# Optimization experiments

Hardware: AMD Instinct MI355X
Metric: run time of the kernel (lower is better)

Reference implementation:

```python
import jax, jax.numpy as jnp
import numpy as np

# irreps_in = irreps_out = 256x0e + 128x1o + 64x2e
MULS = [256, 128, 64]      # multiplicities per irrep
IRDIMS = [1, 3, 5]          # 2l+1 for l=0,1,2
N = 200000                  # number of atoms / nodes
DIM = sum(m * d for m, d in zip(MULS, IRDIMS))          # 960
WNUM = sum(m * m for m in MULS)                          # 86016
BNUM = MULS[0]                                           # bias only on scalar (0e) outputs


def setup_inputs() -> dict:
    key = jax.random.key(0)
    k1, k2, k3 = jax.random.split(key, 3)
    x = jax.random.normal(k1, (N, DIM), dtype=jnp.float32)
    w = jax.random.normal(k2, (WNUM,), dtype=jnp.float32)
    b = jax.random.normal(k3, (BNUM,), dtype=jnp.float32) * 0.1
    return {"x": x, "w": w, "b": b}


def reference(x, w, b):
    # Faithful to _codegen_linear with f_in=f_out=None, shared_weights=True:
    # per-irrep block einsum 'uw,zui->zwi' scaled by 1/sqrt(mul_in), plus bias on 0e block.
    n = x.shape[0]
    outs = []
    xoff = 0
    woff = 0
    for mul, d in zip(MULS, IRDIMS):
        blk = x[:, xoff:xoff + mul * d].reshape(n, mul, d)          # (N, u, i)
        W = w[woff:woff + mul * mul].reshape(mul, mul)              # (u, w)
        pw = mul ** -0.5                                            # path_weight (element norm)
        o = pw * jnp.einsum('uw,nui->nwi', W, blk)                  # (N, w, i)
        o = o.reshape(n, mul * d)
        if d == 1:  # scalar irrep: bias path, path_weight = 1
            o = o + b.reshape(1, mul)
        outs.append(o)
        xoff += mul * d
        woff += mul * mul
    return jnp.concatenate(outs, axis=-1)  # (N, 960)
```

## Files before the change

kernel.cpp:

```cpp
#include <hip/hip_runtime.h>


typedef short frag8 __attribute__((ext_vector_type(8)));
typedef float f32x4 __attribute__((ext_vector_type(4)));
typedef unsigned int u32;
typedef u32 u32x4 __attribute__((ext_vector_type(4)));

static __device__ __forceinline__ short f2bf(float f) {
    union { float f; unsigned u; } v; v.f = f;
    unsigned r = (v.u + 0x7FFFu + ((v.u >> 16) & 1u)) >> 16;
    return (short)r;
}

static __device__ __forceinline__ u32 cvtpk(float lo, float hi) {
    u32 r;
    asm("v_cvt_pk_bf16_f32 %0, %1, %2" : "=v"(r) : "v"(lo), "v"(hi));
    return r;
}

static __device__ __forceinline__ frag8 asfrag(u32x4 u) {
    union { u32x4 u; frag8 f; } t; t.u = u; return t.f;
}

#define MFMA(a, b, c) __builtin_amdgcn_mfma_f32_16x16x32_bf16((a), (b), (c), 0, 0, 0)

__global__ __launch_bounds__(256) void prep_kernel(const float* __restrict__ w,
                                                   short* __restrict__ wf) {
    int e = blockIdx.x * 256 + threadIdx.x;
    int f = e >> 9;
    int r = e & 511;
    int l = r >> 3, j = r & 7;
    int l15 = l & 15, lg = l >> 4;
    int kk = 4 * lg + (j & 3) + 16 * (j >> 2);
    int u, wc, woff, mul; float scale;
    if (f < 128) {
        int nt = f >> 3, s = f & 7;
        u = 32 * s + kk; wc = nt * 16 + l15; woff = 0;     mul = 256; scale = 0.0625f;
    } else if (f < 160) {
        int g = f - 128, nt = g >> 2, s = g & 3;
        u = 32 * s + kk; wc = nt * 16 + l15; woff = 65536; mul = 128; scale = 0.088388347648318447f;
    } else {
        int g = f - 160, nt = g >> 1, s = g & 1;
        u = 32 * s + kk; wc = nt * 16 + l15; woff = 81920; mul = 64;  scale = 0.125f;
    }
    wf[e] = f2bf(scale * w[woff + u * mul + wc]);
}

static __device__ __forceinline__ void gload_lds16(const void* g, void* l) {
    __builtin_amdgcn_global_load_lds(
        (const __attribute__((address_space(1))) unsigned int*)g,
        (__attribute__((address_space(3))) unsigned int*)l, 16, 0, 0);
}

__global__ __launch_bounds__(256) void lin_tile(const float* __restrict__ x,
                                                const short* __restrict__ wf,
                                                const float* __restrict__ bias,
                                                float* __restrict__ out) {
    __shared__ __align__(16) char smem[24576];
    const int tid  = threadIdx.x;
    const int lane = tid & 63;
    const int wv   = tid >> 6;
    const int l15  = lane & 15;
    const int lg   = lane >> 4;
    const int fam  = blockIdx.y;
    const long rowbase = (long)blockIdx.x * 16;
    const char* __restrict__ xb = (const char*)x + rowbase * 3840;
    char* __restrict__ ob = (char*)out + rowbase * 3840;
    const frag8* __restrict__ wfr = (const frag8*)wf;
    const int sw4 = (l15 & 7) << 4;

    if (fam == 0) {
        #pragma unroll
        for (int j = 0; j < 4; ++j) {
            int c  = j * 256 + tid;
            int r  = c >> 6;
            int cc = c & 63;
            int g  = cc ^ (r & 7);
            gload_lds16(xb + r * 3840 + (g << 4),
                        smem + (j * 256 + wv * 64) * 16);
        }
    } else if (fam == 1) {
        #pragma unroll
        for (int j = 0; j < 6; ++j) {
            int c  = j * 256 + tid;
            int r  = c / 96;
            int cc = c - r * 96;
            int g  = cc ^ (r & 7);
            gload_lds16(xb + r * 3840 + 1024 + (g << 4),
                        smem + (j * 256 + wv * 64) * 16);
        }
    } else {
        #pragma unroll
        for (int j = 0; j < 5; ++j) {
            int c  = j * 256 + tid;
            int r  = c / 80;
            int cc = c - r * 80;
            int g  = cc ^ (r & 7);
            gload_lds16(xb + r * 3840 + 2560 + (g << 4),
                        smem + (j * 256 + wv * 64) * 16);
        }
    }
    __syncthreads();

    if (fam == 0) {
        const char* sb = smem + l15 * 1024;
        #define LDC0(cc) (*(const f32x4*)(sb + (((cc) << 4) ^ sw4)))
        frag8 a0[8];
        #pragma unroll
        for (int s = 0; s < 8; ++s) {
            const f32x4 v0 = LDC0(8 * s + lg);
            const f32x4 v1 = LDC0(8 * s + 4 + lg);
            u32x4 t = { cvtpk(v0[0], v0[1]), cvtpk(v0[2], v0[3]),
                        cvtpk(v1[0], v1[1]), cvtpk(v1[2], v1[3]) };
            a0[s] = asfrag(t);
        }
        #undef LDC0
        f32x4 st[4];
        #pragma unroll
        for (int q = 0; q < 4; ++q) {
            const int nt = 4 * wv + q;
            f32x4 acc = {0.f, 0.f, 0.f, 0.f};
            #pragma unroll
            for (int s = 0; s < 8; ++s) {
                frag8 bw = wfr[(nt * 8 + s) * 64 + lane];
                acc = MFMA(bw, a0[s], acc);
            }
            const f32x4 bv = *(const f32x4*)(bias + nt * 16 + 4 * lg);
            st[q][0] = acc[0] + bv[0]; st[q][1] = acc[1] + bv[1];
            st[q][2] = acc[2] + bv[2]; st[q][3] = acc[3] + bv[3];
        }
        __syncthreads();
        #pragma unroll
        for (int q = 0; q < 4; ++q) {
            const int g0 = (4 * wv + q) * 4 + lg;
            *(f32x4*)(smem + l15 * 1024 + (((g0 ^ (l15 & 7))) << 4)) = st[q];
        }
        __syncthreads();
        #pragma unroll
        for (int j = 0; j < 4; ++j) {
            int c = j * 256 + tid;
            int r = c >> 6;
            int g = c & 63;
            f32x4 v = *(const f32x4*)(smem + r * 1024 + ((g ^ (r & 7)) << 4));
            *(f32x4*)(ob + (long)r * 3840 + (g << 4)) = v;
        }
    } else if (fam == 1) {
        const char* sb = smem + l15 * 1536;
        #define LDC1(cc) (*(const f32x4*)(sb + (((cc) << 4) ^ sw4)))
        u32x4 a1u[12];
        #pragma unroll
        for (int s = 0; s < 4; ++s) {
            #pragma unroll
            for (int h = 0; h < 2; ++h) {
                const int cb = 24 * s + 12 * h + 3 * lg;
                const f32x4 q0 = LDC1(cb);
                const f32x4 q1 = LDC1(cb + 1);
                const f32x4 q2 = LDC1(cb + 2);
                a1u[0 + s][2 * h]     = cvtpk(q0[0], q0[3]);
                a1u[0 + s][2 * h + 1] = cvtpk(q1[2], q2[1]);
                a1u[4 + s][2 * h]     = cvtpk(q0[1], q1[0]);
                a1u[4 + s][2 * h + 1] = cvtpk(q1[3], q2[2]);
                a1u[8 + s][2 * h]     = cvtpk(q0[2], q1[1]);
                a1u[8 + s][2 * h + 1] = cvtpk(q2[0], q2[3]);
            }
        }
        #undef LDC1
        f32x4 sv[2][3];
        #pragma unroll
        for (int q = 0; q < 2; ++q) {
            const int nt = 2 * wv + q;
            f32x4 c0 = {0.f,0.f,0.f,0.f}, c1 = {0.f,0.f,0.f,0.f}, c2 = {0.f,0.f,0.f,0.f};
            #pragma unroll
            for (int s = 0; s < 4; ++s) {
                frag8 bw = wfr[(128 + nt * 4 + s) * 64 + lane];
                c0 = MFMA(bw, asfrag(a1u[0 + s]), c0);
                c1 = MFMA(bw, asfrag(a1u[4 + s]), c1);
                c2 = MFMA(bw, asfrag(a1u[8 + s]), c2);
            }
            sv[q][0] = (f32x4){c0[0], c1[0], c2[0], c0[1]};
            sv[q][1] = (f32x4){c1[1], c2[1], c0[2], c1[2]};
            sv[q][2] = (f32x4){c2[2], c0[3], c1[3], c2[3]};
        }
        __syncthreads();
        #pragma unroll
        for (int q = 0; q < 2; ++q) {
            const int g0 = 3 * ((2 * wv + q) * 4 + lg);
            char* wb = smem + l15 * 1536;
            #pragma unroll
            for (int i = 0; i < 3; ++i)
                *(f32x4*)(wb + (((g0 + i) ^ (l15 & 7)) << 4)) = sv[q][i];
        }
        __syncthreads();
        #pragma unroll
        for (int j = 0; j < 6; ++j) {
            int c = j * 256 + tid;
            int r = c / 96;
            int g = c - r * 96;
            f32x4 v = *(const f32x4*)(smem + r * 1536 + ((g ^ (r & 7)) << 4));
            *(f32x4*)(ob + (long)r * 3840 + 1024 + (g << 4)) = v;
        }
    } else {
        const char* sb = smem + l15 * 1280;
        #define LDC2(cc) (*(const f32x4*)(sb + (((cc) << 4) ^ sw4)))
        u32x4 a2u[10];
        #pragma unroll
        for (int s = 0; s < 2; ++s) {
            #pragma unroll
            for (int h = 0; h < 2; ++h) {
                const int cb = 40 * s + 20 * h + 5 * lg;
                const f32x4 q0 = LDC2(cb);
                const f32x4 q1 = LDC2(cb + 1);
                const f32x4 q2 = LDC2(cb + 2);
                const f32x4 q3 = LDC2(cb + 3);
                const f32x4 q4 = LDC2(cb + 4);
                a2u[0 + s][2 * h]     = cvtpk(q0[0], q1[1]);
                a2u[0 + s][2 * h + 1] = cvtpk(q2[2], q3[3]);
                a2u[2 + s][2 * h]     = cvtpk(q0[1], q1[2]);
                a2u[2 + s][2 * h + 1] = cvtpk(q2[3], q4[0]);
                a2u[4 + s][2 * h]     = cvtpk(q0[2], q1[3]);
                a2u[4 + s][2 * h + 1] = cvtpk(q3[0], q4[1]);
                a2u[6 + s][2 * h]     = cvtpk(q0[3], q2[0]);
                a2u[6 + s][2 * h + 1] = cvtpk(q3[1], q4[2]);
                a2u[8 + s][2 * h]     = cvtpk(q1[0], q2[1]);
                a2u[8 + s][2 * h + 1] = cvtpk(q3[2], q4[3]);
            }
        }
        #undef LDC2
        f32x4 sv[5];
        {
            const int nt = wv;
            f32x4 c0 = {0.f,0.f,0.f,0.f}, c1 = {0.f,0.f,0.f,0.f}, c2 = {0.f,0.f,0.f,0.f},
                  c3 = {0.f,0.f,0.f,0.f}, c4 = {0.f,0.f,0.f,0.f};
            #pragma unroll
            for (int s = 0; s < 2; ++s) {
                frag8 bw = wfr[(160 + nt * 2 + s) * 64 + lane];
                c0 = MFMA(bw, asfrag(a2u[0 + s]), c0);
                c1 = MFMA(bw, asfrag(a2u[2 + s]), c1);
                c2 = MFMA(bw, asfrag(a2u[4 + s]), c2);
                c3 = MFMA(bw, asfrag(a2u[6 + s]), c3);
                c4 = MFMA(bw, asfrag(a2u[8 + s]), c4);
            }
            sv[0] = (f32x4){c0[0], c1[0], c2[0], c3[0]};
            sv[1] = (f32x4){c4[0], c0[1], c1[1], c2[1]};
            sv[2] = (f32x4){c3[1], c4[1], c0[2], c1[2]};
            sv[3] = (f32x4){c2[2], c3[2], c4[2], c0[3]};
            sv[4] = (f32x4){c1[3], c2[3], c3[3], c4[3]};
        }
        __syncthreads();
        {
            const int g0 = 5 * (wv * 4 + lg);
            char* wb = smem + l15 * 1280;
            #pragma unroll
            for (int i = 0; i < 5; ++i)
                *(f32x4*)(wb + (((g0 + i) ^ (l15 & 7)) << 4)) = sv[i];
        }
        __syncthreads();
        #pragma unroll
        for (int j = 0; j < 5; ++j) {
            int c = j * 256 + tid;
            int r = c / 80;
            int g = c - r * 80;
            f32x4 v = *(const f32x4*)(smem + r * 1280 + ((g ^ (r & 7)) << 4));
            *(f32x4*)(ob + (long)r * 3840 + 2560 + (g << 4)) = v;
        }
    }
}

extern "C" void kernel_launch(void* const* d_in, const int* in_sizes, int n_in,
                              void* d_out, int out_size, void* d_ws, size_t ws_size,
                              hipStream_t stream) {
    const float* x = (const float*)d_in[0];
    const float* w = (const float*)d_in[1];
    const float* b = (const float*)d_in[2];
    float* out = (float*)d_out;
    short* wf  = (short*)d_ws;

    hipLaunchKernelGGL(prep_kernel, dim3(336), dim3(256), 0, stream, w, wf);
    hipLaunchKernelGGL(lin_tile, dim3(12500, 3), dim3(256), 0, stream,
                       x, wf, b, out);
}
```

Measured before the change: 353.7 us.

## Make blocks persistent over five row tiles with double-buffered async LDS prefetch

Each block now handles five consecutive 16-row tiles instead of one, and prefetches the next tile into a second LDS buffer with global_load_lds while computing the current one. Output staging moves to a separate LDS region. Bias and weight fragments are hoisted into registers once per block. The aim is to overlap global loads with MFMA work and to amortise block launch and weight loads, at the cost of 72KB of dynamic LDS per block, which sharply lowers resident blocks per CU.

```diff
diff --git a/kernel.cpp b/kernel.cpp
--- a/kernel.cpp
+++ b/kernel.cpp
@@ -5,6 +5,8 @@
 typedef float f32x4 __attribute__((ext_vector_type(4)));
 typedef unsigned int u32;
 typedef u32 u32x4 __attribute__((ext_vector_type(4)));
+
+#define TILE_B 61440L
 
 static __device__ __forceinline__ short f2bf(float f) {
     union { float f; unsigned u; } v; v.f = f;
@@ -52,216 +54,251 @@
         (__attribute__((address_space(3))) unsigned int*)l, 16, 0, 0);
 }
 
-__global__ __launch_bounds__(256) void lin_tile(const float* __restrict__ x,
+__global__ __launch_bounds__(256) void lin_pipe(const float* __restrict__ x,
                                                 const short* __restrict__ wf,
                                                 const float* __restrict__ bias,
                                                 float* __restrict__ out) {
-    __shared__ __align__(16) char smem[24576];
+    extern __shared__ __align__(16) char smem[];
     const int tid  = threadIdx.x;
     const int lane = tid & 63;
     const int wv   = tid >> 6;
     const int l15  = lane & 15;
     const int lg   = lane >> 4;
+    const int sw4  = (l15 & 7) << 4;
     const int fam  = blockIdx.y;
-    const long rowbase = (long)blockIdx.x * 16;
-    const char* __restrict__ xb = (const char*)x + rowbase * 3840;
-    char* __restrict__ ob = (char*)out + rowbase * 3840;
+    const long tile0 = (long)blockIdx.x * 5;
+    const char* __restrict__ xbase = (const char*)x;
+    char* __restrict__ obase = (char*)out;
     const frag8* __restrict__ wfr = (const frag8*)wf;
-    const int sw4 = (l15 & 7) << 4;
 
     if (fam == 0) {
-        #pragma unroll
-        for (int j = 0; j < 4; ++j) {
-            int c  = j * 256 + tid;
-            int r  = c >> 6;
-            int cc = c & 63;
-            int g  = cc ^ (r & 7);
-            gload_lds16(xb + r * 3840 + (g << 4),
-                        smem + (j * 256 + wv * 64) * 16);
+        f32x4 bv[4];
+        #pragma unroll
+        for (int q = 0; q < 4; ++q)
+            bv[q] = *(const f32x4*)(bias + (4 * wv + q) * 16 + 4 * lg);
+        {
+            const char* xb = xbase + tile0 * TILE_B;
+            #pragma unroll
+            for (int j = 0; j < 4; ++j) {
+                int c = j * 256 + tid, r = c >> 6, g = (c & 63) ^ (r & 7);
+                gload_lds16(xb + r * 3840 + (g << 4), smem + (j * 256 + wv * 64) * 16);
+            }
+        }
+        __syncthreads();
+        #pragma unroll
+        for (int it = 0; it < 5; ++it) {
+            const long tile = tile0 + it;
+            const int cur = it & 1;
+            if (it < 4) {
+                const char* xb = xbase + (tile + 1) * TILE_B;
+                char* db = smem + (cur ^ 1) * 16384;
+                #pragma unroll
+                for (int j = 0; j < 4; ++j) {
+                    int c = j * 256 + tid, r = c >> 6, g = (c & 63) ^ (r & 7);
+                    gload_lds16(xb + r * 3840 + (g << 4), db + (j * 256 + wv * 64) * 16);
+                }
+            }
+            const char* sb = smem + cur * 16384 + l15 * 1024;
+            frag8 a0[8];
+            #pragma unroll
+            for (int s = 0; s < 8; ++s) {
+                const f32x4 v0 = *(const f32x4*)(sb + (((8 * s + lg) << 4) ^ sw4));
+                const f32x4 v1 = *(const f32x4*)(sb + (((8 * s + 4 + lg) << 4) ^ sw4));
+                u32x4 t = { cvtpk(v0[0], v0[1]), cvtpk(v0[2], v0[3]),
+                            cvtpk(v1[0], v1[1]), cvtpk(v1[2], v1[3]) };
+                a0[s] = asfrag(t);
+            }
+            f32x4 st[4];
+            #pragma unroll
+            for (int q = 0; q < 4; ++q) {
+                const int nt = 4 * wv + q;
+                f32x4 acc = {0.f, 0.f, 0.f, 0.f};
+                #pragma unroll
+                for (int s = 0; s < 8; ++s)
+                    acc = MFMA(wfr[(nt * 8 + s) * 64 + lane], a0[s], acc);
+                st[q] = acc + bv[q];
+            }
+            #pragma unroll
+            for (int q = 0; q < 4; ++q) {
+                const int g0 = (4 * wv + q) * 4 + lg;
+                *(f32x4*)(smem + 32768 + l15 * 1024 + ((g0 ^ (l15 & 7)) << 4)) = st[q];
+            }
+            __syncthreads();
+            char* ob = obase + tile * TILE_B;
+            #pragma unroll
+            for (int j = 0; j < 4; ++j) {
+                int c = j * 256 + tid, r = c >> 6, g = c & 63;
+                f32x4 v = *(const f32x4*)(smem + 32768 + r * 1024 + ((g ^ (r & 7)) << 4));
+                *(f32x4*)(ob + (long)r * 3840 + (g << 4)) = v;
+            }
+            __syncthreads();
         }
     } else if (fam == 1) {
-        #pragma unroll
-        for (int j = 0; j < 6; ++j) {
-            int c  = j * 256 + tid;
-            int r  = c / 96;
-            int cc = c - r * 96;
-            int g  = cc ^ (r & 7);
-            gload_lds16(xb + r * 3840 + 1024 + (g << 4),
-                        smem + (j * 256 + wv * 64) * 16);
+        frag8 w1[8];
+        #pragma unroll
+        for (int q = 0; q < 2; ++q)
+            #pragma unroll
+            for (int s = 0; s < 4; ++s)
+                w1[q * 4 + s] = wfr[(128 + (2 * wv + q) * 4 + s) * 64 + lane];
+        {
+            const char* xb = xbase + tile0 * TILE_B;
+            #pragma unroll
+            for (int j = 0; j < 6; ++j) {
+                int c = j * 256 + tid, r = c / 96, cc = c - r * 96, g = cc ^ (r & 7);
+                gload_lds16(xb + r * 3840 + 1024 + (g << 4), smem + (j * 256 + wv * 64) * 16);
+            }
+        }
+        __syncthreads();
+        #pragma unroll
+        for (int it = 0; it < 5; ++it) {
+            const long tile = tile0 + it;
+            const int cur = it & 1;
+            if (it < 4) {
+                const char* xb = xbase + (tile + 1) * TILE_B;
+                char* db = smem + (cur ^ 1) * 24576;
+                #pragma unroll
+                for (int j = 0; j < 6; ++j) {
+                    int c = j * 256 + tid, r = c / 96, cc = c - r * 96, g = cc ^ (r & 7);
+                    gload_lds16(xb + r * 3840 + 1024 + (g << 4), db + (j * 256 + wv * 64) * 16);
+                }
+            }
+            const char* sb = smem + cur * 24576 + l15 * 1536;
+            u32x4 a1u[12];
+            #pragma unroll
+            for (int s = 0; s < 4; ++s) {
+                #pragma unroll
+                for (int h = 0; h < 2; ++h) {
+                    const int cb = 24 * s + 12 * h + 3 * lg;
+                    const f32x4 q0 = *(const f32x4*)(sb + ((cb << 4) ^ sw4));
+                    const f32x4 q1 = *(const f32x4*)(sb + (((cb + 1) << 4) ^ sw4));
+                    const f32x4 q2 = *(const f32x4*)(sb + (((cb + 2) << 4) ^ sw4));
+                    a1u[0 + s][2 * h]     = cvtpk(q0[0], q0[3]);
+                    a1u[0 + s][2 * h + 1] = cvtpk(q1[2], q2[1]);
+                    a1u[4 + s][2 * h]     = cvtpk(q0[1], q1[0]);
+                    a1u[4 + s][2 * h + 1] = cvtpk(q1[3], q2[2]);
+                    a1u[8 + s][2 * h]     = cvtpk(q0[2], q1[1]);
+                    a1u[8 + s][2 * h + 1] = cvtpk(q2[0], q2[3]);
+                }
+            }
+            f32x4 sv[2][3];
+            #pragma unroll
+            for (int q = 0; q < 2; ++q) {
+                f32x4 c0 = {0.f,0.f,0.f,0.f}, c1 = {0.f,0.f,0.f,0.f}, c2 = {0.f,0.f,0.f,0.f};
+                #pragma unroll
+                for (int s = 0; s < 4; ++s) {
+                    frag8 bw = w1[q * 4 + s];
+                    c0 = MFMA(bw, asfrag(a1u[0 + s]), c0);
+                    c1 = MFMA(bw, asfrag(a1u[4 + s]), c1);
+                    c2 = MFMA(bw, asfrag(a1u[8 + s]), c2);
+                }
+                sv[q][0] = (f32x4){c0[0], c1[0], c2[0], c0[1]};
+                sv[q][1] = (f32x4){c1[1], c2[1], c0[2], c1[2]};
+                sv[q][2] = (f32x4){c2[2], c0[3], c1[3], c2[3]};
+            }
+            #pragma unroll
+            for (int q = 0; q < 2; ++q) {
+                const int g0 = 3 * ((2 * wv + q) * 4 + lg);
+                char* wb = smem + 49152 + l15 * 1536;
+                #pragma unroll
+                for (int i = 0; i < 3; ++i)
+                    *(f32x4*)(wb + (((g0 + i) ^ (l15 & 7)) << 4)) = sv[q][i];
+            }
+            __syncthreads();
+            char* ob = obase + tile * TILE_B;
+            #pragma unroll
+            for (int j = 0; j < 6; ++j) {
+                int c = j * 256 + tid, r = c / 96, g = c - r * 96;
+                f32x4 v = *(const f32x4*)(smem + 49152 + r * 1536 + ((g ^ (r & 7)) << 4));
+                *(f32x4*)(ob + (long)r * 3840 + 1024 + (g << 4)) = v;
+            }
+            __syncthreads();
         }
     } else {
-        #pragma unroll
-        for (int j = 0; j < 5; ++j) {
-            int c  = j * 256 + tid;
-            int r  = c / 80;
-            int cc = c - r * 80;
-            int g  = cc ^ (r & 7);
-            gload_lds16(xb + r * 3840 + 2560 + (g << 4),
-                        smem + (j * 256 + wv * 64) * 16);
-        }
-    }
-    __syncthreads();
-
-    if (fam == 0) {
-        const char* sb = smem + l15 * 1024;
-        #define LDC0(cc) (*(const f32x4*)(sb + (((cc) << 4) ^ sw4)))
-        frag8 a0[8];
-        #pragma unroll
-        for (int s = 0; s < 8; ++s) {
-            const f32x4 v0 = LDC0(8 * s + lg);
-            const f32x4 v1 = LDC0(8 * s + 4 + lg);
-            u32x4 t = { cvtpk(v0[0], v0[1]), cvtpk(v0[2], v0[3]),
-                        cvtpk(v1[0], v1[1]), cvtpk(v1[2], v1[3]) };
-            a0[s] = asfrag(t);
-        }
-        #undef LDC0
-        f32x4 st[4];
-        #pragma unroll
-        for (int q = 0; q < 4; ++q) {
-            const int nt = 4 * wv + q;
-            f32x4 acc = {0.f, 0.f, 0.f, 0.f};
-            #pragma unroll
-            for (int s = 0; s < 8; ++s) {
-                frag8 bw = wfr[(nt * 8 + s) * 64 + lane];
-                acc = MFMA(bw, a0[s], acc);
-            }
-            const f32x4 bv = *(const f32x4*)(bias + nt * 16 + 4 * lg);
-            st[q][0] = acc[0] + bv[0]; st[q][1] = acc[1] + bv[1];
-            st[q][2] = acc[2] + bv[2]; st[q][3] = acc[3] + bv[3];
+        frag8 w2[2];
+        #pragma unroll
+        for (int s = 0; s < 2; ++s)
+            w2[s] = wfr[(160 + wv * 2 + s) * 64 + lane];
+        {
+            const char* xb = xbase + tile0 * TILE_B;
+            #pragma unroll
+            for (int j = 0; j < 5; ++j) {
+                int c = j * 256 + tid, r = c / 80, cc = c - r * 80, g = cc ^ (r & 7);
+                gload_lds16(xb + r * 3840 + 2560 + (g << 4), smem + (j * 256 + wv * 64) * 16);
+            }
         }
         __syncthreads();
         #pragma unroll
-        for (int q = 0; q < 4; ++q) {
-            const int g0 = (4 * wv + q) * 4 + lg;
-            *(f32x4*)(smem + l15 * 1024 + (((g0 ^ (l15 & 7))) << 4)) = st[q];
-        }
-        __syncthreads();
-        #pragma unroll
-        for (int j = 0; j < 4; ++j) {
-            int c = j * 256 + tid;
-            int r = c >> 6;
-            int g = c & 63;
-            f32x4 v = *(const f32x4*)(smem + r * 1024 + ((g ^ (r & 7)) << 4));
-            *(f32x4*)(ob + (long)r * 3840 + (g << 4)) = v;
-        }
-    } else if (fam == 1) {
-        const char* sb = smem + l15 * 1536;
-        #define LDC1(cc) (*(const f32x4*)(sb + (((cc) << 4) ^ sw4)))
-        u32x4 a1u[12];
-        #pragma unroll
-        for (int s = 0; s < 4; ++s) {
-            #pragma unroll
-            for (int h = 0; h < 2; ++h) {
-                const int cb = 24 * s + 12 * h + 3 * lg;
-                const f32x4 q0 = LDC1(cb);
-                const f32x4 q1 = LDC1(cb + 1);
-                const f32x4 q2 = LDC1(cb + 2);
-                a1u[0 + s][2 * h]     = cvtpk(q0[0], q0[3]);
-                a1u[0 + s][2 * h + 1] = cvtpk(q1[2], q2[1]);
-                a1u[4 + s][2 * h]     = cvtpk(q0[1], q1[0]);
-                a1u[4 + s][2 * h + 1] = cvtpk(q1[3], q2[2]);
-                a1u[8 + s][2 * h]     = cvtpk(q0[2], q1[1]);
-                a1u[8 + s][2 * h + 1] = cvtpk(q2[0], q2[3]);
-            }
-        }
-        #undef LDC1
-        f32x4 sv[2][3];
-        #pragma unroll
-        for (int q = 0; q < 2; ++q) {
-            const int nt = 2 * wv + q;
-            f32x4 c0 = {0.f,0.f,0.f,0.f}, c1 = {0.f,0.f,0.f,0.f}, c2 = {0.f,0.f,0.f,0.f};
-            #pragma unroll
-            for (int s = 0; s < 4; ++s) {
-                frag8 bw = wfr[(128 + nt * 4 + s) * 64 + lane];
-                c0 = MFMA(bw, asfrag(a1u[0 + s]), c0);
-                c1 = MFMA(bw, asfrag(a1u[4 + s]), c1);
-                c2 = MFMA(bw, asfrag(a1u[8 + s]), c2);
-            }
-            sv[q][0] = (f32x4){c0[0], c1[0], c2[0], c0[1]};
-            sv[q][1] = (f32x4){c1[1], c2[1], c0[2], c1[2]};
-            sv[q][2] = (f32x4){c2[2], c0[3], c1[3], c2[3]};
-        }
-        __syncthreads();
-        #pragma unroll
-        for (int q = 0; q < 2; ++q) {
-            const int g0 = 3 * ((2 * wv + q) * 4 + lg);
-            char* wb = smem + l15 * 1536;
-            #pragma unroll
-            for (int i = 0; i < 3; ++i)
-                *(f32x4*)(wb + (((g0 + i) ^ (l15 & 7)) << 4)) = sv[q][i];
-        }
-        __syncthreads();
-        #pragma unroll
-        for (int j = 0; j < 6; ++j) {
-            int c = j * 256 + tid;
-            int r = c / 96;
-            int g = c - r * 96;
-            f32x4 v = *(const f32x4*)(smem + r * 1536 + ((g ^ (r & 7)) << 4));
-            *(f32x4*)(ob + (long)r * 3840 + 1024 + (g << 4)) = v;
-        }
-    } else {
-        const char* sb = smem + l15 * 1280;
-        #define LDC2(cc) (*(const f32x4*)(sb + (((cc) << 4) ^ sw4)))
-        u32x4 a2u[10];
-        #pragma unroll
-        for (int s = 0; s < 2; ++s) {
-            #pragma unroll
-            for (int h = 0; h < 2; ++h) {
-                const int cb = 40 * s + 20 * h + 5 * lg;
-                const f32x4 q0 = LDC2(cb);
-                const f32x4 q1 = LDC2(cb + 1);
-                const f32x4 q2 = LDC2(cb + 2);
-                const f32x4 q3 = LDC2(cb + 3);
-                const f32x4 q4 = LDC2(cb + 4);
-                a2u[0 + s][2 * h]     = cvtpk(q0[0], q1[1]);
-                a2u[0 + s][2 * h + 1] = cvtpk(q2[2], q3[3]);
-                a2u[2 + s][2 * h]     = cvtpk(q0[1], q1[2]);
-                a2u[2 + s][2 * h + 1] = cvtpk(q2[3], q4[0]);
-                a2u[4 + s][2 * h]     = cvtpk(q0[2], q1[3]);
-                a2u[4 + s][2 * h + 1] = cvtpk(q3[0], q4[1]);
-                a2u[6 + s][2 * h]     = cvtpk(q0[3], q2[0]);
-                a2u[6 + s][2 * h + 1] = cvtpk(q3[1], q4[2]);
-                a2u[8 + s][2 * h]     = cvtpk(q1[0], q2[1]);
-                a2u[8 + s][2 * h + 1] = cvtpk(q3[2], q4[3]);
-            }
-        }
-        #undef LDC2
-        f32x4 sv[5];
-        {
-            const int nt = wv;
-            f32x4 c0 = {0.f,0.f,0.f,0.f}, c1 = {0.f,0.f,0.f,0.f}, c2 = {0.f,0.f,0.f,0.f},
-                  c3 = {0.f,0.f,0.f,0.f}, c4 = {0.f,0.f,0.f,0.f};
+        for (int it = 0; it < 5; ++it) {
+            const long tile = tile0 + it;
+            const int cur = it & 1;
+            if (it < 4) {
+                const char* xb = xbase + (tile + 1) * TILE_B;
+                char* db = smem + (cur ^ 1) * 20480;
+                #pragma unroll
+                for (int j = 0; j < 5; ++j) {
+                    int c = j * 256 + tid, r = c / 80, cc = c - r * 80, g = cc ^ (r & 7);
+                    gload_lds16(xb + r * 3840 + 2560 + (g << 4), db + (j * 256 + wv * 64) * 16);
+                }
+            }
+            const char* sb = smem + cur * 20480 + l15 * 1280;
+            u32x4 a2u[10];
             #pragma unroll
             for (int s = 0; s < 2; ++s) {
-                frag8 bw = wfr[(160 + nt * 2 + s) * 64 + lane];
-                c0 = MFMA(bw, asfrag(a2u[0 + s]), c0);
-                c1 = MFMA(bw, asfrag(a2u[2 + s]), c1);
-                c2 = MFMA(bw, asfrag(a2u[4 + s]), c2);
-                c3 = MFMA(bw, asfrag(a2u[6 + s]), c3);
-                c4 = MFMA(bw, asfrag(a2u[8 + s]), c4);
-            }
-            sv[0] = (f32x4){c0[0], c1[0], c2[0], c3[0]};
-            sv[1] = (f32x4){c4[0], c0[1], c1[1], c2[1]};
-            sv[2] = (f32x4){c3[1], c4[1], c0[2], c1[2]};
-            sv[3] = (f32x4){c2[2], c3[2], c4[2], c0[3]};
-            sv[4] = (f32x4){c1[3], c2[3], c3[3], c4[3]};
-        }
-        __syncthreads();
-        {
-            const int g0 = 5 * (wv * 4 + lg);
-            char* wb = smem + l15 * 1280;
-            #pragma unroll
-            for (int i = 0; i < 5; ++i)
-                *(f32x4*)(wb + (((g0 + i) ^ (l15 & 7)) << 4)) = sv[i];
-        }
-        __syncthreads();
-        #pragma unroll
-        for (int j = 0; j < 5; ++j) {
-            int c = j * 256 + tid;
-            int r = c / 80;
-            int g = c - r * 80;
-            f32x4 v = *(const f32x4*)(smem + r * 1280 + ((g ^ (r & 7)) << 4));
-            *(f32x4*)(ob + (long)r * 3840 + 2560 + (g << 4)) = v;
+                #pragma unroll
+                for (int h = 0; h < 2; ++h) {
+                    const int cb = 40 * s + 20 * h + 5 * lg;
+                    const f32x4 q0 = *(const f32x4*)(sb + ((cb << 4) ^ sw4));
+                    const f32x4 q1 = *(const f32x4*)(sb + (((cb + 1) << 4) ^ sw4));
+                    const f32x4 q2 = *(const f32x4*)(sb + (((cb + 2) << 4) ^ sw4));
+                    const f32x4 q3 = *(const f32x4*)(sb + (((cb + 3) << 4) ^ sw4));
+                    const f32x4 q4 = *(const f32x4*)(sb + (((cb + 4) << 4) ^ sw4));
+                    a2u[0 + s][2 * h]     = cvtpk(q0[0], q1[1]);
+                    a2u[0 + s][2 * h + 1] = cvtpk(q2[2], q3[3]);
+                    a2u[2 + s][2 * h]     = cvtpk(q0[1], q1[2]);
+                    a2u[2 + s][2 * h + 1] = cvtpk(q2[3], q4[0]);
+                    a2u[4 + s][2 * h]     = cvtpk(q0[2], q1[3]);
+                    a2u[4 + s][2 * h + 1] = cvtpk(q3[0], q4[1]);
+                    a2u[6 + s][2 * h]     = cvtpk(q0[3], q2[0]);
+                    a2u[6 + s][2 * h + 1] = cvtpk(q3[1], q4[2]);
+                    a2u[8 + s][2 * h]     = cvtpk(q1[0], q2[1]);
+                    a2u[8 + s][2 * h + 1] = cvtpk(q3[2], q4[3]);
+                }
+            }
+            f32x4 sv[5];
+            {
+                f32x4 c0 = {0.f,0.f,0.f,0.f}, c1 = {0.f,0.f,0.f,0.f}, c2 = {0.f,0.f,0.f,0.f},
+                      c3 = {0.f,0.f,0.f,0.f}, c4 = {0.f,0.f,0.f,0.f};
+                #pragma unroll
+                for (int s = 0; s < 2; ++s) {
+                    frag8 bw = w2[s];
+                    c0 = MFMA(bw, asfrag(a2u[0 + s]), c0);
+                    c1 = MFMA(bw, asfrag(a2u[2 + s]), c1);
+                    c2 = MFMA(bw, asfrag(a2u[4 + s]), c2);
+                    c3 = MFMA(bw, asfrag(a2u[6 + s]), c3);
+                    c4 = MFMA(bw, asfrag(a2u[8 + s]), c4);
+                }
+                sv[0] = (f32x4){c0[0], c1[0], c2[0], c3[0]};
+                sv[1] = (f32x4){c4[0], c0[1], c1[1], c2[1]};
+                sv[2] = (f32x4){c3[1], c4[1], c0[2], c1[2]};
+                sv[3] = (f32x4){c2[2], c3[2], c4[2], c0[3]};
+                sv[4] = (f32x4){c1[3], c2[3], c3[3], c4[3]};
+            }
+            {
+                const int g0 = 5 * (wv * 4 + lg);
+                char* wb = smem + 40960 + l15 * 1280;
+                #pragma unroll
+                for (int i = 0; i < 5; ++i)
+                    *(f32x4*)(wb + (((g0 + i) ^ (l15 & 7)) << 4)) = sv[i];
+            }
+            __syncthreads();
+            char* ob = obase + tile * TILE_B;
+            #pragma unroll
+            for (int j = 0; j < 5; ++j) {
+                int c = j * 256 + tid, r = c / 80, g = c - r * 80;
+                f32x4 v = *(const f32x4*)(smem + 40960 + r * 1280 + ((g ^ (r & 7)) << 4));
+                *(f32x4*)(ob + (long)r * 3840 + 2560 + (g << 4)) = v;
+            }
+            __syncthreads();
         }
     }
 }
@@ -276,6 +313,9 @@
     short* wf  = (short*)d_ws;
 
     hipLaunchKernelGGL(prep_kernel, dim3(336), dim3(256), 0, stream, w, wf);
-    hipLaunchKernelGGL(lin_tile, dim3(12500, 3), dim3(256), 0, stream,
+
+    (void)hipFuncSetAttribute((const void*)lin_pipe,
+                              hipFuncAttributeMaxDynamicSharedMemorySize, 73728);
+    hipLaunchKernelGGL(lin_pipe, dim3(2500, 3), dim3(256), 73728, stream,
                        x, wf, b, out);
 }
```

After: 364.6 us. 1.03x slower.

## Split fused irrep kernel into three specialized kernels with padded LDS rows

Applied to the files above, without the earlier changes.

Replaces the single kernel that branches on blockIdx.y into three separate kernels, one per irrep block, each sized to its own LDS footprint. The XOR-swizzled LDS layout becomes row padding (stride +16 bytes), which simplifies address math and lets a wave load a full row contiguously. Weight fragments for the l=1 and l=2 blocks are now loaded into registers before the x tile arrives, so their latency overlaps the global-to-LDS copy. In exchange there are three launches instead of one, the three blocks no longer run concurrently within one grid, and padded rows may bring back some bank conflicts.

```diff
diff --git a/kernel.cpp b/kernel.cpp
--- a/kernel.cpp
+++ b/kernel.cpp
@@ -5,6 +5,10 @@
 typedef float f32x4 __attribute__((ext_vector_type(4)));
 typedef unsigned int u32;
 typedef u32 u32x4 __attribute__((ext_vector_type(4)));
+
+#define ST0 1040
+#define ST1 1552
+#define ST2 1296
 
 static __device__ __forceinline__ short f2bf(float f) {
     union { float f; unsigned u; } v; v.f = f;
@@ -52,217 +56,221 @@
         (__attribute__((address_space(3))) unsigned int*)l, 16, 0, 0);
 }
 
-__global__ __launch_bounds__(256) void lin_tile(const float* __restrict__ x,
-                                                const short* __restrict__ wf,
-                                                const float* __restrict__ bias,
-                                                float* __restrict__ out) {
-    __shared__ __align__(16) char smem[24576];
-    const int tid  = threadIdx.x;
-    const int lane = tid & 63;
-    const int wv   = tid >> 6;
-    const int l15  = lane & 15;
-    const int lg   = lane >> 4;
-    const int fam  = blockIdx.y;
+__global__ __launch_bounds__(256) void lin_f0(const float* __restrict__ x,
+                                              const short* __restrict__ wf,
+                                              const float* __restrict__ bias,
+                                              float* __restrict__ out) {
+    __shared__ __align__(16) char smem[16 * ST0];
+    const int tid = threadIdx.x, lane = tid & 63, wv = tid >> 6;
+    const int l15 = lane & 15, lg = lane >> 4;
     const long rowbase = (long)blockIdx.x * 16;
     const char* __restrict__ xb = (const char*)x + rowbase * 3840;
     char* __restrict__ ob = (char*)out + rowbase * 3840;
     const frag8* __restrict__ wfr = (const frag8*)wf;
-    const int sw4 = (l15 & 7) << 4;
-
-    if (fam == 0) {
-        #pragma unroll
-        for (int j = 0; j < 4; ++j) {
-            int c  = j * 256 + tid;
-            int r  = c >> 6;
-            int cc = c & 63;
-            int g  = cc ^ (r & 7);
-            gload_lds16(xb + r * 3840 + (g << 4),
-                        smem + (j * 256 + wv * 64) * 16);
-        }
-    } else if (fam == 1) {
-        #pragma unroll
-        for (int j = 0; j < 6; ++j) {
-            int c  = j * 256 + tid;
-            int r  = c / 96;
-            int cc = c - r * 96;
-            int g  = cc ^ (r & 7);
-            gload_lds16(xb + r * 3840 + 1024 + (g << 4),
-                        smem + (j * 256 + wv * 64) * 16);
-        }
-    } else {
-        #pragma unroll
-        for (int j = 0; j < 5; ++j) {
-            int c  = j * 256 + tid;
-            int r  = c / 80;
-            int cc = c - r * 80;
-            int g  = cc ^ (r & 7);
-            gload_lds16(xb + r * 3840 + 2560 + (g << 4),
-                        smem + (j * 256 + wv * 64) * 16);
-        }
-    }
-    __syncthreads();
-
-    if (fam == 0) {
-        const char* sb = smem + l15 * 1024;
-        #define LDC0(cc) (*(const f32x4*)(sb + (((cc) << 4) ^ sw4)))
-        frag8 a0[8];
-        #pragma unroll
-        for (int s = 0; s < 8; ++s) {
-            const f32x4 v0 = LDC0(8 * s + lg);
-            const f32x4 v1 = LDC0(8 * s + 4 + lg);
-            u32x4 t = { cvtpk(v0[0], v0[1]), cvtpk(v0[2], v0[3]),
-                        cvtpk(v1[0], v1[1]), cvtpk(v1[2], v1[3]) };
-            a0[s] = asfrag(t);
-        }
-        #undef LDC0
-        f32x4 st[4];
-        #pragma unroll
-        for (int q = 0; q < 4; ++q) {
-            const int nt = 4 * wv + q;
-            f32x4 acc = {0.f, 0.f, 0.f, 0.f};
-            #pragma unroll
-            for (int s = 0; s < 8; ++s) {
-                frag8 bw = wfr[(nt * 8 + s) * 64 + lane];
-                acc = MFMA(bw, a0[s], acc);
-            }
-            const f32x4 bv = *(const f32x4*)(bias + nt * 16 + 4 * lg);
-            st[q][0] = acc[0] + bv[0]; st[q][1] = acc[1] + bv[1];
-            st[q][2] = acc[2] + bv[2]; st[q][3] = acc[3] + bv[3];
-        }
-        __syncthreads();
-        #pragma unroll
-        for (int q = 0; q < 4; ++q) {
-            const int g0 = (4 * wv + q) * 4 + lg;
-            *(f32x4*)(smem + l15 * 1024 + (((g0 ^ (l15 & 7))) << 4)) = st[q];
-        }
-        __syncthreads();
-        #pragma unroll
-        for (int j = 0; j < 4; ++j) {
-            int c = j * 256 + tid;
-            int r = c >> 6;
-            int g = c & 63;
-            f32x4 v = *(const f32x4*)(smem + r * 1024 + ((g ^ (r & 7)) << 4));
-            *(f32x4*)(ob + (long)r * 3840 + (g << 4)) = v;
-        }
-    } else if (fam == 1) {
-        const char* sb = smem + l15 * 1536;
-        #define LDC1(cc) (*(const f32x4*)(sb + (((cc) << 4) ^ sw4)))
-        u32x4 a1u[12];
+
+    #pragma unroll
+    for (int r4 = 0; r4 < 4; ++r4) {
+        int r = 4 * wv + r4;
+        gload_lds16(xb + (long)r * 3840 + (long)lane * 16, smem + r * ST0);
+    }
+    __syncthreads();
+
+    const char* sb = smem + l15 * ST0;
+    frag8 a0[8];
+    #pragma unroll
+    for (int s = 0; s < 8; ++s) {
+        const f32x4 v0 = *(const f32x4*)(sb + (8 * s + lg) * 16);
+        const f32x4 v1 = *(const f32x4*)(sb + (8 * s + 4 + lg) * 16);
+        u32x4 t = { cvtpk(v0[0], v0[1]), cvtpk(v0[2], v0[3]),
+                    cvtpk(v1[0], v1[1]), cvtpk(v1[2], v1[3]) };
+        a0[s] = asfrag(t);
+    }
+    f32x4 st[4];
+    #pragma unroll
+    for (int q = 0; q < 4; ++q) {
+        const int nt = 4 * wv + q;
+        f32x4 acc = {0.f, 0.f, 0.f, 0.f};
+        #pragma unroll
+        for (int s = 0; s < 8; ++s)
+            acc = MFMA(wfr[(nt * 8 + s) * 64 + lane], a0[s], acc);
+        const f32x4 bv = *(const f32x4*)(bias + nt * 16 + 4 * lg);
+        st[q] = acc + bv;
+    }
+    __syncthreads();
+    #pragma unroll
+    for (int q = 0; q < 4; ++q) {
+        const int g0 = (4 * wv + q) * 4 + lg;
+        *(f32x4*)(smem + l15 * ST0 + g0 * 16) = st[q];
+    }
+    __syncthreads();
+    #pragma unroll
+    for (int j = 0; j < 4; ++j) {
+        int c = j * 256 + tid, r = c >> 6, g = c & 63;
+        f32x4 v = *(const f32x4*)(smem + r * ST0 + g * 16);
+        *(f32x4*)(ob + (long)r * 3840 + g * 16) = v;
+    }
+}
+
+__global__ __launch_bounds__(256) void lin_f1(const float* __restrict__ x,
+                                              const short* __restrict__ wf,
+                                              float* __restrict__ out) {
+    __shared__ __align__(16) char smem[16 * ST1];
+    const int tid = threadIdx.x, lane = tid & 63, wv = tid >> 6;
+    const int l15 = lane & 15, lg = lane >> 4;
+    const long rowbase = (long)blockIdx.x * 16;
+    const char* __restrict__ xb = (const char*)x + rowbase * 3840;
+    char* __restrict__ ob = (char*)out + rowbase * 3840;
+    const frag8* __restrict__ wfr = (const frag8*)wf;
+
+    frag8 w1[8];
+    #pragma unroll
+    for (int q = 0; q < 2; ++q)
+        #pragma unroll
+        for (int s = 0; s < 4; ++s)
+            w1[q * 4 + s] = wfr[(128 + (2 * wv + q) * 4 + s) * 64 + lane];
+
+    #pragma unroll
+    for (int r4 = 0; r4 < 4; ++r4) {
+        int r = 4 * wv + r4;
+        gload_lds16(xb + (long)r * 3840 + 1024 + (long)lane * 16, smem + r * ST1);
+        if (lane < 32)
+            gload_lds16(xb + (long)r * 3840 + 2048 + (long)lane * 16,
+                        smem + r * ST1 + 1024);
+    }
+    __syncthreads();
+
+    const char* sb = smem + l15 * ST1;
+    u32x4 a1u[12];
+    #pragma unroll
+    for (int s = 0; s < 4; ++s) {
+        #pragma unroll
+        for (int h = 0; h < 2; ++h) {
+            const int cb = 24 * s + 12 * h + 3 * lg;
+            const f32x4 q0 = *(const f32x4*)(sb + (cb    ) * 16);
+            const f32x4 q1 = *(const f32x4*)(sb + (cb + 1) * 16);
+            const f32x4 q2 = *(const f32x4*)(sb + (cb + 2) * 16);
+            a1u[0 + s][2 * h]     = cvtpk(q0[0], q0[3]);
+            a1u[0 + s][2 * h + 1] = cvtpk(q1[2], q2[1]);
+            a1u[4 + s][2 * h]     = cvtpk(q0[1], q1[0]);
+            a1u[4 + s][2 * h + 1] = cvtpk(q1[3], q2[2]);
+            a1u[8 + s][2 * h]     = cvtpk(q0[2], q1[1]);
+            a1u[8 + s][2 * h + 1] = cvtpk(q2[0], q2[3]);
+        }
+    }
+    f32x4 sv[2][3];
+    #pragma unroll
+    for (int q = 0; q < 2; ++q) {
+        f32x4 c0 = {0.f,0.f,0.f,0.f}, c1 = {0.f,0.f,0.f,0.f}, c2 = {0.f,0.f,0.f,0.f};
         #pragma unroll
         for (int s = 0; s < 4; ++s) {
-            #pragma unroll
-            for (int h = 0; h < 2; ++h) {
-                const int cb = 24 * s + 12 * h + 3 * lg;
-                const f32x4 q0 = LDC1(cb);
-                const f32x4 q1 = LDC1(cb + 1);
-                const f32x4 q2 = LDC1(cb + 2);
-                a1u[0 + s][2 * h]     = cvtpk(q0[0], q0[3]);
-                a1u[0 + s][2 * h + 1] = cvtpk(q1[2], q2[1]);
-                a1u[4 + s][2 * h]     = cvtpk(q0[1], q1[0]);
-                a1u[4 + s][2 * h + 1] = cvtpk(q1[3], q2[2]);
-                a1u[8 + s][2 * h]     = cvtpk(q0[2], q1[1]);
-                a1u[8 + s][2 * h + 1] = cvtpk(q2[0], q2[3]);
-            }
-        }
-        #undef LDC1
-        f32x4 sv[2][3];
-        #pragma unroll
-        for (int q = 0; q < 2; ++q) {
-            const int nt = 2 * wv + q;
-            f32x4 c0 = {0.f,0.f,0.f,0.f}, c1 = {0.f,0.f,0.f,0.f}, c2 = {0.f,0.f,0.f,0.f};
-            #pragma unroll
-            for (int s = 0; s < 4; ++s) {
-                frag8 bw = wfr[(128 + nt * 4 + s) * 64 + lane];
-                c0 = MFMA(bw, asfrag(a1u[0 + s]), c0);
-                c1 = MFMA(bw, asfrag(a1u[4 + s]), c1);
-                c2 = MFMA(bw, asfrag(a1u[8 + s]), c2);
-            }
-            sv[q][0] = (f32x4){c0[0], c1[0], c2[0], c0[1]};
-            sv[q][1] = (f32x4){c1[1], c2[1], c0[2], c1[2]};
-            sv[q][2] = (f32x4){c2[2], c0[3], c1[3], c2[3]};
-        }
-        __syncthreads();
-        #pragma unroll
-        for (int q = 0; q < 2; ++q) {
-            const int g0 = 3 * ((2 * wv + q) * 4 + lg);
-            char* wb = smem + l15 * 1536;
-            #pragma unroll
-            for (int i = 0; i < 3; ++i)
-                *(f32x4*)(wb + (((g0 + i) ^ (l15 & 7)) << 4)) = sv[q][i];
-        }
-        __syncthreads();
-        #pragma unroll
-        for (int j = 0; j < 6; ++j) {
-            int c = j * 256 + tid;
-            int r = c / 96;
-            int g = c - r * 96;
-            f32x4 v = *(const f32x4*)(smem + r * 1536 + ((g ^ (r & 7)) << 4));
-            *(f32x4*)(ob + (long)r * 3840 + 1024 + (g << 4)) = v;
-        }
-    } else {
-        const char* sb = smem + l15 * 1280;
-        #define LDC2(cc) (*(const f32x4*)(sb + (((cc) << 4) ^ sw4)))
-        u32x4 a2u[10];
+            frag8 bw = w1[q * 4 + s];
+            c0 = MFMA(bw, asfrag(a1u[0 + s]), c0);
+            c1 = MFMA(bw, asfrag(a1u[4 + s]), c1);
+            c2 = MFMA(bw, asfrag(a1u[8 + s]), c2);
+        }
+        sv[q][0] = (f32x4){c0[0], c1[0], c2[0], c0[1]};
+        sv[q][1] = (f32x4){c1[1], c2[1], c0[2], c1[2]};
+        sv[q][2] = (f32x4){c2[2], c0[3], c1[3], c2[3]};
+    }
+    __syncthreads();
+    #pragma unroll
+    for (int q = 0; q < 2; ++q) {
+        const int g0 = 3 * ((2 * wv + q) * 4 + lg);
+        #pragma unroll
+        for (int i = 0; i < 3; ++i)
+            *(f32x4*)(smem + l15 * ST1 + (g0 + i) * 16) = sv[q][i];
+    }
+    __syncthreads();
+    #pragma unroll
+    for (int j = 0; j < 6; ++j) {
+        int c = j * 256 + tid, r = c / 96, g = c - r * 96;
+        f32x4 v = *(const f32x4*)(smem + r * ST1 + g * 16);
+        *(f32x4*)(ob + (long)r * 3840 + 1024 + g * 16) = v;
+    }
+}
+
+__global__ __launch_bounds__(256) void lin_f2(const float* __restrict__ x,
+                                              const short* __restrict__ wf,
+                                              float* __restrict__ out) {
+    __shared__ __align__(16) char smem[16 * ST2];
+    const int tid = threadIdx.x, lane = tid & 63, wv = tid >> 6;
+    const int l15 = lane & 15, lg = lane >> 4;
+    const long rowbase = (long)blockIdx.x * 16;
+    const char* __restrict__ xb = (const char*)x + rowbase * 3840;
+    char* __restrict__ ob = (char*)out + rowbase * 3840;
+    const frag8* __restrict__ wfr = (const frag8*)wf;
+
+    frag8 w2[2];
+    #pragma unroll
+    for (int s = 0; s < 2; ++s)
+        w2[s] = wfr[(160 + wv * 2 + s) * 64 + lane];
+
+    #pragma unroll
+    for (int r4 = 0; r4 < 4; ++r4) {
+        int r = 4 * wv + r4;
+        gload_lds16(xb + (long)r * 3840 + 2560 + (long)lane * 16, smem + r * ST2);
+        if (lane < 16)
+            gload_lds16(xb + (long)r * 3840 + 3584 + (long)lane * 16,
+                        smem + r * ST2 + 1024);
+    }
+    __syncthreads();
+
+    const char* sb = smem + l15 * ST2;
+    u32x4 a2u[10];
+    #pragma unroll
+    for (int s = 0; s < 2; ++s) {
+        #pragma unroll
+        for (int h = 0; h < 2; ++h) {
+            const int cb = 40 * s + 20 * h + 5 * lg;
+            const f32x4 q0 = *(const f32x4*)(sb + (cb    ) * 16);
+            const f32x4 q1 = *(const f32x4*)(sb + (cb + 1) * 16);
+            const f32x4 q2 = *(const f32x4*)(sb + (cb + 2) * 16);
+            const f32x4 q3 = *(const f32x4*)(sb + (cb + 3) * 16);
+            const f32x4 q4 = *(const f32x4*)(sb + (cb + 4) * 16);
+            a2u[0 + s][2 * h]     = cvtpk(q0[0], q1[1]);
+            a2u[0 + s][2 * h + 1] = cvtpk(q2[2], q3[3]);
+            a2u[2 + s][2 * h]     = cvtpk(q0[1], q1[2]);
+            a2u[2 + s][2 * h + 1] = cvtpk(q2[3], q4[0]);
+            a2u[4 + s][2 * h]     = cvtpk(q0[2], q1[3]);
+            a2u[4 + s][2 * h + 1] = cvtpk(q3[0], q4[1]);
+            a2u[6 + s][2 * h]     = cvtpk(q0[3], q2[0]);
+            a2u[6 + s][2 * h + 1] = cvtpk(q3[1], q4[2]);
+            a2u[8 + s][2 * h]     = cvtpk(q1[0], q2[1]);
+            a2u[8 + s][2 * h + 1] = cvtpk(q3[2], q4[3]);
+        }
+    }
+    f32x4 sv[5];
+    {
+        f32x4 c0 = {0.f,0.f,0.f,0.f}, c1 = {0.f,0.f,0.f,0.f}, c2 = {0.f,0.f,0.f,0.f},
+              c3 = {0.f,0.f,0.f,0.f}, c4 = {0.f,0.f,0.f,0.f};
         #pragma unroll
         for (int s = 0; s < 2; ++s) {
-            #pragma unroll
-            for (int h = 0; h < 2; ++h) {
-                const int cb = 40 * s + 20 * h + 5 * lg;
-                const f32x4 q0 = LDC2(cb);
-                const f32x4 q1 = LDC2(cb + 1);
-                const f32x4 q2 = LDC2(cb + 2);
-                const f32x4 q3 = LDC2(cb + 3);
-                const f32x4 q4 = LDC2(cb + 4);
-                a2u[0 + s][2 * h]     = cvtpk(q0[0], q1[1]);
-                a2u[0 + s][2 * h + 1] = cvtpk(q2[2], q3[3]);
-                a2u[2 + s][2 * h]     = cvtpk(q0[1], q1[2]);
-                a2u[2 + s][2 * h + 1] = cvtpk(q2[3], q4[0]);
-                a2u[4 + s][2 * h]     = cvtpk(q0[2], q1[3]);
-                a2u[4 + s][2 * h + 1] = cvtpk(q3[0], q4[1]);
-                a2u[6 + s][2 * h]     = cvtpk(q0[3], q2[0]);
-                a2u[6 + s][2 * h + 1] = cvtpk(q3[1], q4[2]);
-                a2u[8 + s][2 * h]     = cvtpk(q1[0], q2[1]);
-                a2u[8 + s][2 * h + 1] = cvtpk(q3[2], q4[3]);
-            }
-        }
-        #undef LDC2
-        f32x4 sv[5];
-        {
-            const int nt = wv;
-            f32x4 c0 = {0.f,0.f,0.f,0.f}, c1 = {0.f,0.f,0.f,0.f}, c2 = {0.f,0.f,0.f,0.f},
-                  c3 = {0.f,0.f,0.f,0.f}, c4 = {0.f,0.f,0.f,0.f};
-            #pragma unroll
-            for (int s = 0; s < 2; ++s) {
-                frag8 bw = wfr[(160 + nt * 2 + s) * 64 + lane];
-                c0 = MFMA(bw, asfrag(a2u[0 + s]), c0);
-                c1 = MFMA(bw, asfrag(a2u[2 + s]), c1);
-                c2 = MFMA(bw, asfrag(a2u[4 + s]), c2);
-                c3 = MFMA(bw, asfrag(a2u[6 + s]), c3);
-                c4 = MFMA(bw, asfrag(a2u[8 + s]), c4);
-            }
-            sv[0] = (f32x4){c0[0], c1[0], c2[0], c3[0]};
-            sv[1] = (f32x4){c4[0], c0[1], c1[1], c2[1]};
-            sv[2] = (f32x4){c3[1], c4[1], c0[2], c1[2]};
-            sv[3] = (f32x4){c2[2], c3[2], c4[2], c0[3]};
-            sv[4] = (f32x4){c1[3], c2[3], c3[3], c4[3]};
-        }
-        __syncthreads();
-        {
-            const int g0 = 5 * (wv * 4 + lg);
-            char* wb = smem + l15 * 1280;
-            #pragma unroll
-            for (int i = 0; i < 5; ++i)
-                *(f32x4*)(wb + (((g0 + i) ^ (l15 & 7)) << 4)) = sv[i];
-        }
-        __syncthreads();
-        #pragma unroll
-        for (int j = 0; j < 5; ++j) {
-            int c = j * 256 + tid;
-            int r = c / 80;
-            int g = c - r * 80;
-            f32x4 v = *(const f32x4*)(smem + r * 1280 + ((g ^ (r & 7)) << 4));
-            *(f32x4*)(ob + (long)r * 3840 + 2560 + (g << 4)) = v;
-        }
+            frag8 bw = w2[s];
+            c0 = MFMA(bw, asfrag(a2u[0 + s]), c0);
+            c1 = MFMA(bw, asfrag(a2u[2 + s]), c1);
+            c2 = MFMA(bw, asfrag(a2u[4 + s]), c2);
+            c3 = MFMA(bw, asfrag(a2u[6 + s]), c3);
+            c4 = MFMA(bw, asfrag(a2u[8 + s]), c4);
+        }
+        sv[0] = (f32x4){c0[0], c1[0], c2[0], c3[0]};
+        sv[1] = (f32x4){c4[0], c0[1], c1[1], c2[1]};
+        sv[2] = (f32x4){c3[1], c4[1], c0[2], c1[2]};
+        sv[3] = (f32x4){c2[2], c3[2], c4[2], c0[3]};
+        sv[4] = (f32x4){c1[3], c2[3], c3[3], c4[3]};
+    }
+    __syncthreads();
+    {
+        const int g0 = 5 * (wv * 4 + lg);
+        #pragma unroll
+        for (int i = 0; i < 5; ++i)
+            *(f32x4*)(smem + l15 * ST2 + (g0 + i) * 16) = sv[i];
+    }
+    __syncthreads();
+    #pragma unroll
+    for (int j = 0; j < 5; ++j) {
+        int c = j * 256 + tid, r = c / 80, g = c - r * 80;
+        f32x4 v = *(const f32x4*)(smem + r * ST2 + g * 16);
+        *(f32x4*)(ob + (long)r * 3840 + 2560 + g * 16) = v;
     }
 }
 
@@ -276,6 +284,7 @@
     short* wf  = (short*)d_ws;
 
     hipLaunchKernelGGL(prep_kernel, dim3(336), dim3(256), 0, stream, w, wf);
-    hipLaunchKernelGGL(lin_tile, dim3(12500, 3), dim3(256), 0, stream,
-                       x, wf, b, out);
-}
+    hipLaunchKernelGGL(lin_f0, dim3(12500), dim3(256), 0, stream, x, wf, b, out);
+    hipLaunchKernelGGL(lin_f1, dim3(12500), dim3(256), 0, stream, x, wf, out);
+    hipLaunchKernelGGL(lin_f2, dim3(12500), dim3(256), 0, stream, x, wf, out);
+}
```

Result: no change. 359.0 us (+1.5%).
